# Kernel optimization log

Measured on AMD Instinct MI355X. Metric: run time of the kernel, lower is better.

The kernel has to match this reference:

```python
import jax, jax.numpy as jnp
import numpy as np

NE, NM, D = 10000, 2048, 128
LEVELS = 6  # levels arg 5 -> self.levels = 6 relation types


def setup_inputs() -> dict:
    key = jax.random.key(0)
    ks = jax.random.split(key, 9)
    s = 0.05
    return {
        "emb_entity": jax.random.normal(ks[0], (1, NE, D), jnp.float32),
        "emb_mole": jax.random.normal(ks[1], (1, NM, D), jnp.float32),
        "entity_mole_weight": jax.random.uniform(ks[2], (NE, NM), jnp.float32),
        "W1": jax.random.normal(ks[3], (LEVELS, D, D), jnp.float32) * s,
        "root1": jax.random.normal(ks[4], (D, D), jnp.float32) * s,
        "b1": jax.random.normal(ks[5], (D,), jnp.float32) * s,
        "W2": jax.random.normal(ks[6], (LEVELS, D, D), jnp.float32) * s,
        "root2": jax.random.normal(ks[7], (D, D), jnp.float32) * s,
        "b2": jax.random.normal(ks[8], (D,), jnp.float32) * s,
    }


def reference(emb_entity, emb_mole, entity_mole_weight, W1, root1, b1, W2, root2, b2):
    x_e = emb_entity[0]  # [NE, D]
    x_m = emb_mole[0]    # [NM, D]
    # weight w in (i/LEVELS, (i+1)/LEVELS]  <=>  ceil(w*LEVELS) - 1 == i ; only i=1..LEVELS-1 form edges
    lev = jnp.ceil(entity_mole_weight * LEVELS).astype(jnp.int32) - 1  # [NE, NM]

    def rel_agg(x_src, W):
        # RGCN mean aggregation per relation type (edges Mole -> Entity), summed over relations
        out = jnp.zeros((x_e.shape[0], W.shape[-1]), x_src.dtype)
        for r in range(1, LEVELS):
            mask = (lev == r).astype(x_src.dtype)          # [NE, NM] relation-r adjacency
            cnt = mask.sum(axis=1, keepdims=True)          # in-degree per entity for relation r
            inv = jnp.where(cnt > 0, 1.0 / cnt, 0.0)
            out = out + ((mask @ x_src) * inv) @ W[r]      # mean message then relation transform
        return out

    # conv1 over homogeneous graph [Entity; Mole]; moles receive no edges -> root+bias only
    e1 = x_e @ root1 + rel_agg(x_m, W1) + b1
    m1 = x_m @ root1 + b1
    e1 = jax.nn.relu(e1)
    m1 = jax.nn.relu(m1)
    # conv2; only the entity slice of the output is returned
    e2 = e1 @ root2 + rel_agg(m1, W2) + b2
    return e2[None]  # [1, NE, D]
```

## Files before the change

### kernel.cpp

```cpp
#include <hip/hip_runtime.h>
#include <stdint.h>


#define NE 10000
#define NM 2048
#define NEPAD 10112
#define MB128 79
#define KSPLIT 16

typedef short bf8_t __attribute__((ext_vector_type(8)));
typedef float f16f  __attribute__((ext_vector_type(16)));

__device__ __forceinline__ uint16_t f2bf(float f){
  uint32_t u = __float_as_uint(f);
  u += 0x7FFFu + ((u >> 16) & 1u);
  return (uint16_t)(u >> 16);
}

__device__ __forceinline__ f16f mfma32(bf8_t a, bf8_t b, f16f c){
  return __builtin_amdgcn_mfma_f32_32x32x16_bf16(a, b, c, 0, 0, 0);
}

__global__ __launch_bounds__(256) void k_init(
    const float* __restrict__ w, const float* __restrict__ xe,
    const float* __restrict__ xm, const float* __restrict__ root1,
    const float* __restrict__ W1, const float* __restrict__ b1,
    uint32_t* __restrict__ levq, float* __restrict__ inv,
    uint16_t* __restrict__ xebf, uint16_t* __restrict__ m1,
    uint16_t* __restrict__ z1){
  int t = threadIdx.x;
  int lane = t & 63, wid = t >> 6;
  int l31 = lane & 31, g = lane >> 5;

  if (blockIdx.x >= 316){
    int gb = blockIdx.x - 316;
    int gbx = gb & 15, gby = gb >> 4;
    bool m1path = (gby == 0);
    const float* Bsrc = m1path ? root1 : (W1 + (size_t)gby*16384);
    int arow = gbx*128 + wid*32 + l31;

    f16f acc[4];
    #pragma unroll
    for (int n = 0; n < 4; n++)
      #pragma unroll
      for (int i = 0; i < 16; i++) acc[n][i] = 0.f;

    #pragma unroll
    for (int ksI = 0; ksI < 8; ksI++){
      int k0 = ksI*16 + g*8;
      const float* ap = xm + (size_t)arow*128 + k0;
      float4 f0 = *(const float4*)ap;
      float4 f1 = *(const float4*)(ap + 4);
      union { uint16_t u[8]; bf8_t v; } ua;
      ua.u[0]=f2bf(f0.x); ua.u[1]=f2bf(f0.y); ua.u[2]=f2bf(f0.z); ua.u[3]=f2bf(f0.w);
      ua.u[4]=f2bf(f1.x); ua.u[5]=f2bf(f1.y); ua.u[6]=f2bf(f1.z); ua.u[7]=f2bf(f1.w);
      #pragma unroll
      for (int n = 0; n < 4; n++){
        int d = n*32 + l31;
        union { uint16_t u[8]; bf8_t v; } ub;
        #pragma unroll
        for (int e = 0; e < 8; e++)
          ub.u[e] = f2bf(Bsrc[(size_t)(k0+e)*128 + d]);
        acc[n] = mfma32(ua.v, ub.v, acc[n]);
      }
    }
    #pragma unroll
    for (int n = 0; n < 4; n++){
      int colg = n*32 + l31;
      float bv = m1path ? b1[colg] : 0.f;
      #pragma unroll
      for (int v = 0; v < 16; v++){
        int rowl = (v&3) + 8*(v>>2) + 4*g;
        int rg = gbx*128 + wid*32 + rowl;
        float val = acc[n][v];
        if (m1path){
          m1[(size_t)rg*128 + colg] = f2bf(fmaxf(val + bv, 0.f));
        } else {
          int pos = ((rg & 1) << 2) | ((rg & 7) >> 1);
          z1[(size_t)((gby-1)*256 + (rg>>3))*1024 + colg*8 + pos] = f2bf(val);
        }
      }
    }
    return;
  }

  int brow = blockIdx.x * 32;
  int rloc = t >> 3, p = t & 7;
  int row = brow + rloc;
  bool active = row < NE;
  const float* wr = w + (size_t)row * NM;
  unsigned long long cnt = 0ull;
  __shared__ uint32_t tile[32][33];

  for (int cp = 0; cp < 8; cp++){
    uint32_t packs[4];
    #pragma unroll
    for (int q = 0; q < 4; q++){
      int gck = cp*32 + p + 8*q;
      uint32_t L = 0;
      if (active){
        const float4* f = (const float4*)(wr + gck*8);
        float4 f0 = f[0], f1 = f[1];
        float wv[8] = {f0.x,f0.y,f0.z,f0.w, f1.x,f1.y,f1.z,f1.w};
        #pragma unroll
        for (int e = 0; e < 8; e++){
          int s = (int)ceilf(wv[e]*6.0f);
          if (s >= 2) cnt += 1ull << (12*(s-2));
          L |= (uint32_t)s << (4*e);
        }
      }
      packs[q] = L;
    }
    __syncthreads();
    #pragma unroll
    for (int q = 0; q < 4; q++) tile[p + 8*q][rloc] = packs[q];
    __syncthreads();
    int ckk = t >> 3;
    int r4  = (t & 7) * 4;
    size_t base = (size_t)(cp*32 + ckk) * NEPAD + brow + r4;
    *(uint4*)(levq + base) = make_uint4(tile[ckk][r4], tile[ckk][r4+1],
                                        tile[ckk][r4+2], tile[ckk][r4+3]);
  }

  unsigned long long c = cnt;
  c += __shfl_xor(c, 1);
  c += __shfl_xor(c, 2);
  c += __shfl_xor(c, 4);
  if (p == 0 && row < NEPAD){
    if (active){
      inv[row*8 + 0] = 0.f; inv[row*8 + 6] = 0.f; inv[row*8 + 7] = 0.f;
      #pragma unroll
      for (int r = 1; r <= 5; r++){
        uint32_t cc = (uint32_t)((c >> (12*(r-1))) & 0xFFFull);
        inv[row*8 + r] = cc ? 1.0f/(float)cc : 0.f;
      }
    } else {
      #pragma unroll
      for (int i = 0; i < 8; i++) inv[row*8 + i] = 0.f;
    }
  }

  int f0i = p * 16;
  if (active){
    union { uint16_t u[16]; uint4 q[2]; } ub;
    #pragma unroll
    for (int j = 0; j < 4; j++){
      float4 a = *(const float4*)(xe + (size_t)row*128 + f0i + j*4);
      ub.u[j*4+0]=f2bf(a.x); ub.u[j*4+1]=f2bf(a.y); ub.u[j*4+2]=f2bf(a.z); ub.u[j*4+3]=f2bf(a.w);
    }
    *(uint4*)(xebf + (size_t)row*128 + f0i)     = ub.q[0];
    *(uint4*)(xebf + (size_t)row*128 + f0i + 8) = ub.q[1];
  } else if (row < NEPAD){
    uint4 z = make_uint4(0,0,0,0);
    *(uint4*)(xebf + (size_t)row*128 + f0i)     = z;
    *(uint4*)(xebf + (size_t)row*128 + f0i + 8) = z;
  }
}

template<bool S16, bool ROOT>
__device__ __forceinline__ void conv_core(
    const uint32_t* __restrict__ levq, const float* __restrict__ inv,
    const uint16_t* __restrict__ zpk, const uint16_t* __restrict__ aroot,
    const float* __restrict__ rootf,
    uint16_t* __restrict__ p16, float* __restrict__ p32, int tid){
  int lane = tid & 63, wid = tid >> 6;
  int l31 = lane & 31, g = lane >> 5;
  int wm = wid >> 1, wn = wid & 1;
  int brow = blockIdx.x*128;
  int ks = blockIdx.y;
  int kc0 = ks*16;
  int rowA = brow + wm*64 + l31;
  int rowB = rowA + 32;
  int colb = wn*64;

  uint32_t LA[8], LB[8];
  #pragma unroll
  for (int kk = 0; kk < 8; kk++){
    int kt = kc0 + kk*2 + g;
    LA[kk] = levq[(size_t)kt*NEPAD + rowA];
    LB[kk] = levq[(size_t)kt*NEPAD + rowB];
  }

  uint32_t tlo[2][5], thi[2][5];
  #pragma unroll
  for (int mt = 0; mt < 2; mt++){
    int rg = mt ? rowB : rowA;
    #pragma unroll
    for (int r = 1; r <= 5; r++){
      uint32_t bits = (uint32_t)f2bf(inv[(size_t)rg*8 + r]);
      int sh = 8*((r+1)&3);
      tlo[mt][r-1] = (bits & 0xFFu) << sh;
      thi[mt][r-1] = (bits >> 8)    << sh;
    }
  }

  f16f acc[2][2];
  #pragma unroll
  for (int a0=0;a0<2;a0++)
    #pragma unroll
    for (int b0=0;b0<2;b0++)
      #pragma unroll
      for (int i=0;i<16;i++) acc[a0][b0][i]=0.f;

  if (ROOT && ks < 8){
    int k0 = ks*16 + g*8;
    bf8_t a0 = *(const bf8_t*)(aroot + (size_t)rowA*128 + k0);
    bf8_t a1 = *(const bf8_t*)(aroot + (size_t)rowB*128 + k0);
    #pragma unroll
    for (int nt = 0; nt < 2; nt++){
      int d = colb + nt*32 + l31;
      union { uint16_t u[8]; bf8_t v; } ub;
      #pragma unroll
      for (int e = 0; e < 8; e++)
        ub.u[e] = f2bf(rootf[(size_t)(k0+e)*128 + d]);
      acc[0][nt] = mfma32(a0, ub.v, acc[0][nt]);
      acc[1][nt] = mfma32(a1, ub.v, acc[1][nt]);
    }
  }

  #pragma unroll
  for (int kk = 0; kk < 8; kk++){
    int kt = kc0 + kk*2 + g;
    uint32_t sxA = LA[kk] & 0x0F0F0F0Fu, syA = (LA[kk] >> 4) & 0x0F0F0F0Fu;
    uint32_t sxB = LB[kk] & 0x0F0F0F0Fu, syB = (LB[kk] >> 4) & 0x0F0F0F0Fu;
    const uint16_t* zb = zpk + (size_t)kt*1024 + (size_t)(colb + l31)*8;
    #pragma unroll
    for (int r = 1; r <= 5; r++){
      const uint16_t* zr = zb + (size_t)(r-1)*262144;
      bf8_t bn0 = *(const bf8_t*)(zr);
      bf8_t bn1 = *(const bf8_t*)(zr + 256);
      #pragma unroll
      for (int mt = 0; mt < 2; mt++){
        uint32_t sx = mt ? sxB : sxA;
        uint32_t sy = mt ? syB : syA;
        uint32_t TL = tlo[mt][r-1], TH = thi[mt][r-1];
        uint32_t pl, ph, ql, qh;
        if (r < 3){
          pl = __builtin_amdgcn_perm(0u, TL, sx);
          ph = __builtin_amdgcn_perm(0u, TH, sx);
          ql = __builtin_amdgcn_perm(0u, TL, sy);
          qh = __builtin_amdgcn_perm(0u, TH, sy);
        } else {
          pl = __builtin_amdgcn_perm(TL, 0u, sx);
          ph = __builtin_amdgcn_perm(TH, 0u, sx);
          ql = __builtin_amdgcn_perm(TL, 0u, sy);
          qh = __builtin_amdgcn_perm(TH, 0u, sy);
        }
        union { uint32_t u[4]; bf8_t v; } A;
        A.u[0] = __builtin_amdgcn_perm(ph, pl, 0x05010400u);
        A.u[1] = __builtin_amdgcn_perm(ph, pl, 0x07030602u);
        A.u[2] = __builtin_amdgcn_perm(qh, ql, 0x05010400u);
        A.u[3] = __builtin_amdgcn_perm(qh, ql, 0x07030602u);
        acc[mt][0] = mfma32(A.v, bn0, acc[mt][0]);
        acc[mt][1] = mfma32(A.v, bn1, acc[mt][1]);
      }
    }
  }

  if (S16){
    uint16_t* dst = p16 + (size_t)ks*NEPAD*128;
    #pragma unroll
    for (int mt = 0; mt < 2; mt++){
      #pragma unroll
      for (int nt = 0; nt < 2; nt++){
        int colg = colb + nt*32 + l31;
        #pragma unroll
        for (int v = 0; v < 16; v++){
          int rowl = (v&3) + 8*(v>>2) + 4*g;
          dst[(size_t)(brow + wm*64 + mt*32 + rowl)*128 + colg] = f2bf(acc[mt][nt][v]);
        }
      }
    }
  } else {
    #pragma unroll
    for (int mt = 0; mt < 2; mt++){
      #pragma unroll
      for (int nt = 0; nt < 2; nt++){
        int colg = colb + nt*32 + l31;
        #pragma unroll
        for (int v = 0; v < 16; v++){
          int rowl = (v&3) + 8*(v>>2) + 4*g;
          unsafeAtomicAdd(&p32[(size_t)(brow + wm*64 + mt*32 + rowl)*128 + colg],
                          acc[mt][nt][v]);
        }
      }
    }
  }
}

template<bool S16>
__global__ __launch_bounds__(256, 3) void k_convA(
    const uint32_t* __restrict__ levq, const float* __restrict__ inv,
    const uint16_t* __restrict__ z1, const uint16_t* __restrict__ xebf,
    const float* __restrict__ root1,
    const uint16_t* __restrict__ m1, const float* __restrict__ W2,
    uint16_t* __restrict__ z2,
    uint16_t* __restrict__ p16, float* __restrict__ p32){
  int tid = threadIdx.x;
  int lane = tid & 63, wid = tid >> 6;
  int l31 = lane & 31, g = lane >> 5;

  if (blockIdx.x >= MB128){
    int fb = blockIdx.y*5 + (blockIdx.x - MB128);
    int r = fb >> 4;
    int rowb = (fb & 15)*128 + wid*32;
    int arow = rowb + l31;
    const float* Bsrc = W2 + (size_t)(r+1)*16384;
    f16f acc[4];
    #pragma unroll
    for (int n = 0; n < 4; n++)
      #pragma unroll
      for (int i = 0; i < 16; i++) acc[n][i] = 0.f;
    #pragma unroll
    for (int ksI = 0; ksI < 8; ksI++){
      int k0 = ksI*16 + g*8;
      bf8_t a = *(const bf8_t*)(m1 + (size_t)arow*128 + k0);
      #pragma unroll
      for (int n = 0; n < 4; n++){
        int d = n*32 + l31;
        union { uint16_t u[8]; bf8_t v; } ub;
        #pragma unroll
        for (int e = 0; e < 8; e++)
          ub.u[e] = f2bf(Bsrc[(size_t)(k0+e)*128 + d]);
        acc[n] = mfma32(a, ub.v, acc[n]);
      }
    }
    #pragma unroll
    for (int n = 0; n < 4; n++){
      int colg = n*32 + l31;
      #pragma unroll
      for (int v = 0; v < 16; v++){
        int rowl = (v&3) + 8*(v>>2) + 4*g;
        int rg = rowb + rowl;
        int pos = ((rg & 1) << 2) | ((rg & 7) >> 1);
        z2[(size_t)(r*256 + (rg>>3))*1024 + colg*8 + pos] = f2bf(acc[n][v]);
      }
    }
    return;
  }
  conv_core<S16, true>(levq, inv, z1, xebf, root1, p16, p32, tid);
}

template<bool S16>
__global__ __launch_bounds__(256, 3) void k_convB(
    const uint32_t* __restrict__ levq, const float* __restrict__ inv,
    const uint16_t* __restrict__ z2,
    const uint16_t* __restrict__ pA16, const float* __restrict__ pA32,
    const float* __restrict__ root2, const float* __restrict__ b1,
    uint16_t* __restrict__ pB16, float* __restrict__ pB32,
    float* __restrict__ rootslab){
  __shared__ uint16_t e1s[128*136];
  int tid = threadIdx.x;
  int lane = tid & 63, wid = tid >> 6;
  int l31 = lane & 31, g = lane >> 5;

  if (blockIdx.x >= MB128){
    int rid = blockIdx.y*5 + (blockIdx.x - MB128);
    if (rid >= MB128) return;
    #pragma unroll
    for (int c = 0; c < 8; c++){
      int eo = c*2048 + tid*8;
      size_t base = (size_t)rid*16384 + eo;
      int col = eo & 127;
      float s[8];
      float4 bv0 = *(const float4*)(b1 + col);
      float4 bv1 = *(const float4*)(b1 + col + 4);
      s[0]=bv0.x; s[1]=bv0.y; s[2]=bv0.z; s[3]=bv0.w;
      s[4]=bv1.x; s[5]=bv1.y; s[6]=bv1.z; s[7]=bv1.w;
      if (S16){
        #pragma unroll
        for (int sl = 0; sl < KSPLIT; sl++){
          union { uint4 q; uint16_t h[8]; } u;
          u.q = *(const uint4*)(pA16 + (size_t)sl*NEPAD*128 + base);
          #pragma unroll
          for (int j = 0; j < 8; j++) s[j] += __uint_as_float(((uint32_t)u.h[j]) << 16);
        }
      } else {
        #pragma unroll
        for (int j = 0; j < 8; j += 4){
          float4 v = *(const float4*)(pA32 + base + j);
          s[j] += v.x; s[j+1] += v.y; s[j+2] += v.z; s[j+3] += v.w;
        }
      }
      union { uint16_t u[8]; uint4 q; } ub;
      #pragma unroll
      for (int j = 0; j < 8; j++) ub.u[j] = f2bf(fmaxf(s[j], 0.f));
      int row = eo >> 7;
      *(uint4*)(&e1s[row*136 + col]) = ub.q;
    }
    __syncthreads();
    f16f racc[4];
    #pragma unroll
    for (int n = 0; n < 4; n++)
      #pragma unroll
      for (int i = 0; i < 16; i++) racc[n][i] = 0.f;
    #pragma unroll
    for (int kk = 0; kk < 8; kk++){
      int k0 = kk*16 + g*8;
      bf8_t a = *(const bf8_t*)(&e1s[(wid*32 + l31)*136 + k0]);
      #pragma unroll
      for (int n = 0; n < 4; n++){
        int d = n*32 + l31;
        union { uint16_t u[8]; bf8_t v; } ub;
        #pragma unroll
        for (int e = 0; e < 8; e++)
          ub.u[e] = f2bf(root2[(size_t)(k0+e)*128 + d]);
        racc[n] = mfma32(a, ub.v, racc[n]);
      }
    }
    #pragma unroll
    for (int n = 0; n < 4; n++){
      int colg = n*32 + l31;
      #pragma unroll
      for (int v = 0; v < 16; v++){
        int rowl = (v&3) + 8*(v>>2) + 4*g;
        rootslab[(size_t)(rid*128 + wid*32 + rowl)*128 + colg] = racc[n][v];
      }
    }
    return;
  }
  conv_core<S16, false>(levq, inv, z2, (const uint16_t*)nullptr,
                        (const float*)nullptr, pB16, pB32, tid);
}

template<bool S16>
__global__ __launch_bounds__(256) void k_red2(
    const uint16_t* __restrict__ pB16, const float* __restrict__ pB32,
    const float* __restrict__ rootslab, const float* __restrict__ b2,
    float* __restrict__ out){
  size_t idx8 = ((size_t)blockIdx.x*256 + threadIdx.x) * 8;
  if (idx8 >= (size_t)NE*128) return;
  int col = (int)(idx8 & 127);
  float s[8];
  float4 bv0 = *(const float4*)(b2 + col);
  float4 bv1 = *(const float4*)(b2 + col + 4);
  s[0]=bv0.x; s[1]=bv0.y; s[2]=bv0.z; s[3]=bv0.w;
  s[4]=bv1.x; s[5]=bv1.y; s[6]=bv1.z; s[7]=bv1.w;
  float4 r0 = *(const float4*)(rootslab + idx8);
  float4 r1 = *(const float4*)(rootslab + idx8 + 4);
  s[0]+=r0.x; s[1]+=r0.y; s[2]+=r0.z; s[3]+=r0.w;
  s[4]+=r1.x; s[5]+=r1.y; s[6]+=r1.z; s[7]+=r1.w;
  if (S16){
    #pragma unroll
    for (int sl = 0; sl < KSPLIT; sl++){
      union { uint4 q; uint16_t h[8]; } u;
      u.q = *(const uint4*)(pB16 + (size_t)sl*NEPAD*128 + idx8);
      #pragma unroll
      for (int j = 0; j < 8; j++) s[j] += __uint_as_float(((uint32_t)u.h[j]) << 16);
    }
  } else {
    #pragma unroll
    for (int j = 0; j < 8; j += 4){
      float4 v = *(const float4*)(pB32 + idx8 + j);
      s[j] += v.x; s[j+1] += v.y; s[j+2] += v.z; s[j+3] += v.w;
    }
  }
  *(float4*)(out + idx8)     = make_float4(s[0], s[1], s[2], s[3]);
  *(float4*)(out + idx8 + 4) = make_float4(s[4], s[5], s[6], s[7]);
}

extern "C" void kernel_launch(void* const* d_in, const int* in_sizes, int n_in,
                              void* d_out, int out_size, void* d_ws, size_t ws_size,
                              hipStream_t stream){
  const float* xe  = (const float*)d_in[0];
  const float* xm  = (const float*)d_in[1];
  const float* w   = (const float*)d_in[2];
  const float* W1  = (const float*)d_in[3];
  const float* r1  = (const float*)d_in[4];
  const float* b1  = (const float*)d_in[5];
  const float* W2  = (const float*)d_in[6];
  const float* r2  = (const float*)d_in[7];
  const float* b2  = (const float*)d_in[8];
  float* out = (float*)d_out;
  char* ws = (char*)d_ws;

  constexpr size_t OFF_INV  = 0;
  constexpr size_t OFF_XEBF = OFF_INV  + (size_t)NEPAD*8*4;
  constexpr size_t OFF_M1   = OFF_XEBF + (size_t)NEPAD*128*2;
  constexpr size_t OFF_Z1   = OFF_M1   + (size_t)NM*128*2;
  constexpr size_t OFF_Z2   = OFF_Z1   + (size_t)5*NM*128*2;
  constexpr size_t OFF_LEVQ = OFF_Z2   + (size_t)5*NM*128*2;
  constexpr size_t OFF_PA   = OFF_LEVQ + (size_t)256*NEPAD*4;
  constexpr size_t SLAB16   = (size_t)NEPAD*128*2;
  constexpr size_t SLABF    = (size_t)NEPAD*128*4;
  constexpr size_t OFF_PB   = OFF_PA   + (size_t)KSPLIT*SLAB16;
  constexpr size_t OFF_ROOT = OFF_PB   + (size_t)KSPLIT*SLAB16;
  constexpr size_t NEED_A   = OFF_ROOT + SLABF;
  constexpr size_t OFF_PB_B   = OFF_PA + SLABF;
  constexpr size_t OFF_ROOT_B = OFF_PB_B + SLABF;

  float*    inv  = (float*)   (ws + OFF_INV);
  uint16_t* xebf = (uint16_t*)(ws + OFF_XEBF);
  uint16_t* m1   = (uint16_t*)(ws + OFF_M1);
  uint16_t* z1   = (uint16_t*)(ws + OFF_Z1);
  uint16_t* z2   = (uint16_t*)(ws + OFF_Z2);
  uint32_t* levq = (uint32_t*)(ws + OFF_LEVQ);

  bool tierA = (ws_size >= NEED_A);

  hipLaunchKernelGGL(k_init, dim3(316 + 96), dim3(256), 0, stream,
                     w, xe, xm, r1, W1, b1, levq, inv, xebf, m1, z1);
  if (tierA){
    uint16_t* pA   = (uint16_t*)(ws + OFF_PA);
    uint16_t* pB   = (uint16_t*)(ws + OFF_PB);
    float*    root = (float*)   (ws + OFF_ROOT);
    hipLaunchKernelGGL((k_convA<true>), dim3(MB128 + 5, KSPLIT), dim3(256), 0, stream,
                       levq, inv, z1, xebf, r1, m1, W2, z2, pA, (float*)nullptr);
    hipLaunchKernelGGL((k_convB<true>), dim3(MB128 + 5, KSPLIT), dim3(256), 0, stream,
                       levq, inv, z2, pA, (const float*)nullptr, r2, b1,
                       pB, (float*)nullptr, root);
    hipLaunchKernelGGL((k_red2<true>), dim3((NE*128 + 2047)/2048), dim3(256), 0, stream,
                       pB, (const float*)nullptr, root, b2, out);
  } else {
    float* pA   = (float*)(ws + OFF_PA);
    float* pB   = (float*)(ws + OFF_PB_B);
    float* root = (float*)(ws + OFF_ROOT_B);
    hipMemsetAsync(pA, 0, SLABF, stream);
    hipMemsetAsync(pB, 0, SLABF, stream);
    hipLaunchKernelGGL((k_convA<false>), dim3(MB128 + 5, KSPLIT), dim3(256), 0, stream,
                       levq, inv, z1, xebf, r1, m1, W2, z2, (uint16_t*)nullptr, pA);
    hipLaunchKernelGGL((k_convB<false>), dim3(MB128 + 5, KSPLIT), dim3(256), 0, stream,
                       levq, inv, z2, (const uint16_t*)nullptr, pA, r2, b1,
                       (uint16_t*)nullptr, pB, root);
    hipLaunchKernelGGL((k_red2<false>), dim3((NE*128 + 2047)/2048), dim3(256), 0, stream,
                       (const uint16_t*)nullptr, pB, root, b2, out);
  }
}
```

Baseline: 111.4 us.

## Use 2-wave blocks with each wave computing 128 rows by 64 columns

The conv core changes from 4 waves in a 2x2 arrangement (64x64 per wave) to 2 waves each covering all 128 rows and 64 columns, with 128-thread blocks. Each wave now reuses every loaded B fragment across four M tiles, which halves B-fragment loads per MFMA. The level words and inverse counts are held per M tile, and the TL/TH byte tables are rebuilt inside the loop to save registers. The side work (W2 transform, e1 reduction plus root2) is re-split into 64-row chunks to match the smaller blocks. The cost is more accumulator and level registers per wave and fewer waves per block, which could reduce occupancy and latency hiding.

```diff
diff --git a/kernel.cpp b/kernel.cpp
--- a/kernel.cpp
+++ b/kernel.cpp
@@ -165,38 +165,32 @@
     uint16_t* __restrict__ p16, float* __restrict__ p32, int tid){
   int lane = tid & 63, wid = tid >> 6;
   int l31 = lane & 31, g = lane >> 5;
-  int wm = wid >> 1, wn = wid & 1;
   int brow = blockIdx.x*128;
   int ks = blockIdx.y;
   int kc0 = ks*16;
-  int rowA = brow + wm*64 + l31;
-  int rowB = rowA + 32;
-  int colb = wn*64;
-
-  uint32_t LA[8], LB[8];
+  int colb = wid*64;
+
+  uint32_t L[8][4];
   #pragma unroll
   for (int kk = 0; kk < 8; kk++){
     int kt = kc0 + kk*2 + g;
-    LA[kk] = levq[(size_t)kt*NEPAD + rowA];
-    LB[kk] = levq[(size_t)kt*NEPAD + rowB];
-  }
-
-  uint32_t tlo[2][5], thi[2][5];
+    #pragma unroll
+    for (int mt = 0; mt < 4; mt++)
+      L[kk][mt] = levq[(size_t)kt*NEPAD + brow + mt*32 + l31];
+  }
+
+  uint32_t binv[4][5];
   #pragma unroll
-  for (int mt = 0; mt < 2; mt++){
-    int rg = mt ? rowB : rowA;
-    #pragma unroll
-    for (int r = 1; r <= 5; r++){
-      uint32_t bits = (uint32_t)f2bf(inv[(size_t)rg*8 + r]);
-      int sh = 8*((r+1)&3);
-      tlo[mt][r-1] = (bits & 0xFFu) << sh;
-      thi[mt][r-1] = (bits >> 8)    << sh;
-    }
-  }
-
-  f16f acc[2][2];
+  for (int mt = 0; mt < 4; mt++){
+    int rg = brow + mt*32 + l31;
+    #pragma unroll
+    for (int r = 1; r <= 5; r++)
+      binv[mt][r-1] = (uint32_t)f2bf(inv[(size_t)rg*8 + r]);
+  }
+
+  f16f acc[4][2];
   #pragma unroll
-  for (int a0=0;a0<2;a0++)
+  for (int a0=0;a0<4;a0++)
     #pragma unroll
     for (int b0=0;b0<2;b0++)
       #pragma unroll
@@ -204,8 +198,10 @@
 
   if (ROOT && ks < 8){
     int k0 = ks*16 + g*8;
-    bf8_t a0 = *(const bf8_t*)(aroot + (size_t)rowA*128 + k0);
-    bf8_t a1 = *(const bf8_t*)(aroot + (size_t)rowB*128 + k0);
+    bf8_t am[4];
+    #pragma unroll
+    for (int mt = 0; mt < 4; mt++)
+      am[mt] = *(const bf8_t*)(aroot + (size_t)(brow + mt*32 + l31)*128 + k0);
     #pragma unroll
     for (int nt = 0; nt < 2; nt++){
       int d = colb + nt*32 + l31;
@@ -213,27 +209,30 @@
       #pragma unroll
       for (int e = 0; e < 8; e++)
         ub.u[e] = f2bf(rootf[(size_t)(k0+e)*128 + d]);
-      acc[0][nt] = mfma32(a0, ub.v, acc[0][nt]);
-      acc[1][nt] = mfma32(a1, ub.v, acc[1][nt]);
-    }
-  }
+      #pragma unroll
+      for (int mt = 0; mt < 4; mt++)
+        acc[mt][nt] = mfma32(am[mt], ub.v, acc[mt][nt]);
+    }
+  }
+
+  const uint16_t* zbase = zpk + (size_t)(colb + l31)*8;
 
   #pragma unroll
   for (int kk = 0; kk < 8; kk++){
     int kt = kc0 + kk*2 + g;
-    uint32_t sxA = LA[kk] & 0x0F0F0F0Fu, syA = (LA[kk] >> 4) & 0x0F0F0F0Fu;
-    uint32_t sxB = LB[kk] & 0x0F0F0F0Fu, syB = (LB[kk] >> 4) & 0x0F0F0F0Fu;
-    const uint16_t* zb = zpk + (size_t)kt*1024 + (size_t)(colb + l31)*8;
     #pragma unroll
     for (int r = 1; r <= 5; r++){
-      const uint16_t* zr = zb + (size_t)(r-1)*262144;
+      const uint16_t* zr = zbase + (size_t)((r-1)*256 + kt)*1024;
       bf8_t bn0 = *(const bf8_t*)(zr);
       bf8_t bn1 = *(const bf8_t*)(zr + 256);
       #pragma unroll
-      for (int mt = 0; mt < 2; mt++){
-        uint32_t sx = mt ? sxB : sxA;
-        uint32_t sy = mt ? syB : syA;
-        uint32_t TL = tlo[mt][r-1], TH = thi[mt][r-1];
+      for (int mt = 0; mt < 4; mt++){
+        uint32_t sx = L[kk][mt] & 0x0F0F0F0Fu;
+        uint32_t sy = (L[kk][mt] >> 4) & 0x0F0F0F0Fu;
+        uint32_t bits = binv[mt][r-1];
+        const int sh = 8*((r+1)&3);
+        uint32_t TL = (bits & 0xFFu) << sh;
+        uint32_t TH = (bits >> 8)    << sh;
         uint32_t pl, ph, ql, qh;
         if (r < 3){
           pl = __builtin_amdgcn_perm(0u, TL, sx);
@@ -260,27 +259,27 @@
   if (S16){
     uint16_t* dst = p16 + (size_t)ks*NEPAD*128;
     #pragma unroll
-    for (int mt = 0; mt < 2; mt++){
+    for (int mt = 0; mt < 4; mt++){
       #pragma unroll
       for (int nt = 0; nt < 2; nt++){
         int colg = colb + nt*32 + l31;
         #pragma unroll
         for (int v = 0; v < 16; v++){
           int rowl = (v&3) + 8*(v>>2) + 4*g;
-          dst[(size_t)(brow + wm*64 + mt*32 + rowl)*128 + colg] = f2bf(acc[mt][nt][v]);
+          dst[(size_t)(brow + mt*32 + rowl)*128 + colg] = f2bf(acc[mt][nt][v]);
         }
       }
     }
   } else {
     #pragma unroll
-    for (int mt = 0; mt < 2; mt++){
+    for (int mt = 0; mt < 4; mt++){
       #pragma unroll
       for (int nt = 0; nt < 2; nt++){
         int colg = colb + nt*32 + l31;
         #pragma unroll
         for (int v = 0; v < 16; v++){
           int rowl = (v&3) + 8*(v>>2) + 4*g;
-          unsafeAtomicAdd(&p32[(size_t)(brow + wm*64 + mt*32 + rowl)*128 + colg],
+          unsafeAtomicAdd(&p32[(size_t)(brow + mt*32 + rowl)*128 + colg],
                           acc[mt][nt][v]);
         }
       }
@@ -289,7 +288,7 @@
 }
 
 template<bool S16>
-__global__ __launch_bounds__(256, 3) void k_convA(
+__global__ __launch_bounds__(128, 2) void k_convA(
     const uint32_t* __restrict__ levq, const float* __restrict__ inv,
     const uint16_t* __restrict__ z1, const uint16_t* __restrict__ xebf,
     const float* __restrict__ root1,
@@ -301,9 +300,9 @@
   int l31 = lane & 31, g = lane >> 5;
 
   if (blockIdx.x >= MB128){
-    int fb = blockIdx.y*5 + (blockIdx.x - MB128);
-    int r = fb >> 4;
-    int rowb = (fb & 15)*128 + wid*32;
+    int fb = blockIdx.y*10 + (blockIdx.x - MB128);
+    int r = fb >> 5;
+    int rowb = (fb & 31)*64 + wid*32;
     int arow = rowb + l31;
     const float* Bsrc = W2 + (size_t)(r+1)*16384;
     f16f acc[4];
@@ -342,25 +341,25 @@
 }
 
 template<bool S16>
-__global__ __launch_bounds__(256, 3) void k_convB(
+__global__ __launch_bounds__(128, 2) void k_convB(
     const uint32_t* __restrict__ levq, const float* __restrict__ inv,
     const uint16_t* __restrict__ z2,
     const uint16_t* __restrict__ pA16, const float* __restrict__ pA32,
     const float* __restrict__ root2, const float* __restrict__ b1,
     uint16_t* __restrict__ pB16, float* __restrict__ pB32,
     float* __restrict__ rootslab){
-  __shared__ uint16_t e1s[128*136];
+  __shared__ uint16_t e1s[64*136];
   int tid = threadIdx.x;
   int lane = tid & 63, wid = tid >> 6;
   int l31 = lane & 31, g = lane >> 5;
 
   if (blockIdx.x >= MB128){
-    int rid = blockIdx.y*5 + (blockIdx.x - MB128);
-    if (rid >= MB128) return;
+    int rid = blockIdx.y*10 + (blockIdx.x - MB128);
+    if (rid >= 158) return;
     #pragma unroll
     for (int c = 0; c < 8; c++){
-      int eo = c*2048 + tid*8;
-      size_t base = (size_t)rid*16384 + eo;
+      int eo = c*1024 + tid*8;
+      size_t base = (size_t)rid*8192 + eo;
       int col = eo & 127;
       float s[8];
       float4 bv0 = *(const float4*)(b1 + col);
@@ -414,7 +413,7 @@
       #pragma unroll
       for (int v = 0; v < 16; v++){
         int rowl = (v&3) + 8*(v>>2) + 4*g;
-        rootslab[(size_t)(rid*128 + wid*32 + rowl)*128 + colg] = racc[n][v];
+        rootslab[(size_t)(rid*64 + wid*32 + rowl)*128 + colg] = racc[n][v];
       }
     }
     return;
@@ -504,9 +503,9 @@
     uint16_t* pA   = (uint16_t*)(ws + OFF_PA);
     uint16_t* pB   = (uint16_t*)(ws + OFF_PB);
     float*    root = (float*)   (ws + OFF_ROOT);
-    hipLaunchKernelGGL((k_convA<true>), dim3(MB128 + 5, KSPLIT), dim3(256), 0, stream,
+    hipLaunchKernelGGL((k_convA<true>), dim3(MB128 + 10, KSPLIT), dim3(128), 0, stream,
                        levq, inv, z1, xebf, r1, m1, W2, z2, pA, (float*)nullptr);
-    hipLaunchKernelGGL((k_convB<true>), dim3(MB128 + 5, KSPLIT), dim3(256), 0, stream,
+    hipLaunchKernelGGL((k_convB<true>), dim3(MB128 + 10, KSPLIT), dim3(128), 0, stream,
                        levq, inv, z2, pA, (const float*)nullptr, r2, b1,
                        pB, (float*)nullptr, root);
     hipLaunchKernelGGL((k_red2<true>), dim3((NE*128 + 2047)/2048), dim3(256), 0, stream,
@@ -517,9 +516,9 @@
     float* root = (float*)(ws + OFF_ROOT_B);
     hipMemsetAsync(pA, 0, SLABF, stream);
     hipMemsetAsync(pB, 0, SLABF, stream);
-    hipLaunchKernelGGL((k_convA<false>), dim3(MB128 + 5, KSPLIT), dim3(256), 0, stream,
+    hipLaunchKernelGGL((k_convA<false>), dim3(MB128 + 10, KSPLIT), dim3(128), 0, stream,
                        levq, inv, z1, xebf, r1, m1, W2, z2, (uint16_t*)nullptr, pA);
-    hipLaunchKernelGGL((k_convB<false>), dim3(MB128 + 5, KSPLIT), dim3(256), 0, stream,
+    hipLaunchKernelGGL((k_convB<false>), dim3(MB128 + 10, KSPLIT), dim3(128), 0, stream,
                        levq, inv, z2, (const uint16_t*)nullptr, pA, r2, b1,
                        (uint16_t*)nullptr, pB, root);
     hipLaunchKernelGGL((k_red2<false>), dim3((NE*128 + 2047)/2048), dim3(256), 0, stream,
```

After: 121.6 us. 9.1% more time.
